# Kernel tuning notes

Hardware: AMD Instinct MI355X
Metric: run time of the kernel (lower is better)

## Reference

```python
import jax, jax.numpy as jnp
import numpy as np

N_NODES = 100000
N_EDGES = 600000
FEAT = 128
N_RELS = 8


def setup_inputs() -> dict:
    key = jax.random.key(0)
    k1, k2, k3, k4, k5, k6, k7 = jax.random.split(key, 7)
    return {
        "h": jax.random.normal(k1, (N_NODES, FEAT), dtype=jnp.float32),
        "weight": jax.random.normal(k2, (N_RELS, FEAT, FEAT), dtype=jnp.float32) * (1.0 / np.sqrt(FEAT)),
        "gate_weight": jax.random.normal(k3, (N_RELS, FEAT, 1), dtype=jnp.float32) * (1.0 / np.sqrt(FEAT)),
        "norm": jax.random.uniform(k4, (N_EDGES, 1), dtype=jnp.float32),
        "src": jax.random.randint(k5, (N_EDGES,), 0, N_NODES, dtype=jnp.int32),
        "dst": jax.random.randint(k6, (N_EDGES,), 0, N_NODES, dtype=jnp.int32),
        "rel_type": jax.random.randint(k7, (N_EDGES,), 0, N_RELS, dtype=jnp.int32),
    }


def reference(h, weight, gate_weight, norm, src, dst, rel_type):
    # Transform every node by every relation once: [N, R, F].
    # Mathematically identical to per-edge bmm h_src @ W[rel], but avoids
    # materializing an [E, F, F] gathered weight tensor.
    h_all = jnp.einsum('nd,rdf->nrf', h, weight)            # [N, R, F]
    gate_all = jnp.einsum('nd,rdo->nro', h, gate_weight)[..., 0]  # [N, R]

    msg = h_all[src, rel_type] * norm                        # [E, F]
    gate = jax.nn.sigmoid(gate_all[src, rel_type])[:, None]  # [E, 1]
    msg = msg * gate

    out = jax.ops.segment_sum(msg, dst, num_segments=h.shape[0])  # scatter-sum to dst nodes
    return jax.nn.relu(out)
```

## Files before the change

kernel.cpp:

```cpp
#include <hip/hip_runtime.h>
#include <hip/hip_bf16.h>

#define FEAT 128
#define NRELS 8
#define KTOT 1024
#define BN 32
#define SCAN2 1024

typedef __bf16 bf16_t;
typedef __bf16 bf16x2_t __attribute__((ext_vector_type(2)));
typedef __bf16 bf16x4_t __attribute__((ext_vector_type(4)));
typedef __bf16 bf16x8_t __attribute__((ext_vector_type(8)));
typedef float f32x4 __attribute__((ext_vector_type(4)));

struct __align__(8) PackedEdge { int row; float scale; };

static inline size_t align256(size_t x) { return (x + 255) & ~(size_t)255; }

__global__ void k_convert_w2(const float* __restrict__ w, bf16_t* __restrict__ wt2) {
    int i = blockIdx.x * blockDim.x + threadIdx.x;
    if (i >= NRELS * FEAT * FEAT) return;
    int r = i >> 14;
    int rem = i & 16383;
    int d = rem >> 7;
    int f = rem & 127;
    wt2[(size_t)f * KTOT + r * FEAT + d] = (bf16_t)w[i];
}

__global__ __launch_bounds__(256) void k_prep(const float* __restrict__ h,
                                              const float* __restrict__ gw,
                                              float* __restrict__ sg,
                                              bf16_t* __restrict__ hb, int ncount) {
    int wv = (int)((blockIdx.x * blockDim.x + threadIdx.x) >> 6);
    int lane = threadIdx.x & 63;
    if (wv >= ncount) return;

    float2 hv2 = *reinterpret_cast<const float2*>(h + (size_t)wv * FEAT + lane * 2);
    bf16x2_t hc;
    hc.x = (bf16_t)hv2.x;
    hc.y = (bf16_t)hv2.y;
    *reinterpret_cast<bf16x2_t*>(hb + (size_t)wv * FEAT + lane * 2) = hc;

    int r = lane >> 3;
    int g = lane & 7;
    const float4* hp = reinterpret_cast<const float4*>(h + (size_t)wv * FEAT + g * 16);
    const float4* wp = reinterpret_cast<const float4*>(gw + r * FEAT + g * 16);
    float s = 0.f;
#pragma unroll
    for (int i = 0; i < 4; ++i) {
        float4 a = hp[i];
        float4 b = wp[i];
        s += a.x * b.x + a.y * b.y + a.z * b.z + a.w * b.w;
    }
    s += __shfl_xor(s, 1, 64);
    s += __shfl_xor(s, 2, 64);
    s += __shfl_xor(s, 4, 64);
    if (g == 0) sg[(size_t)wv * NRELS + r] = 1.0f / (1.0f + __expf(-s));
}

__global__ void k_degree8(const int* __restrict__ dstv, const int* __restrict__ rel,
                          int* __restrict__ deg8, int nedges) {
    int e = blockIdx.x * blockDim.x + threadIdx.x;
    if (e >= nedges) return;
    atomicAdd(&deg8[(dstv[e] << 3) | rel[e]], 1);
}

__global__ __launch_bounds__(1024) void k_scan_block2(const int* __restrict__ in,
                                                      int* __restrict__ outv,
                                                      int* __restrict__ bsum, int n) {
    __shared__ int sm[1024];
    int t = threadIdx.x;
    int idx = blockIdx.x * SCAN2 + t;
    int v = (idx < n) ? in[idx] : 0;
    sm[t] = v;
    __syncthreads();
    for (int off = 1; off < 1024; off <<= 1) {
        int x = (t >= off) ? sm[t - off] : 0;
        __syncthreads();
        sm[t] += x;
        __syncthreads();
    }
    if (idx < n) outv[idx] = sm[t] - v;
    if (t == 1023) bsum[blockIdx.x] = sm[1023];
}

__global__ __launch_bounds__(1024) void k_scan_tops(int* __restrict__ bsum, int nb,
                                                    int* __restrict__ rowptr_end) {
    __shared__ int sm[1024];
    int t = threadIdx.x;
    if (nb <= 1024) {
        int v = (t < nb) ? bsum[t] : 0;
        sm[t] = v;
        __syncthreads();
        for (int off = 1; off < 1024; off <<= 1) {
            int x = (t >= off) ? sm[t - off] : 0;
            __syncthreads();
            sm[t] += x;
            __syncthreads();
        }
        if (t < nb) bsum[t] = sm[t] - v;
        if (t == 1023) *rowptr_end = sm[1023];
    } else if (t == 0) {
        int run = 0;
        for (int b = 0; b < nb; ++b) { int v = bsum[b]; bsum[b] = run; run += v; }
        *rowptr_end = run;
    }
}

__global__ void k_scan_add2(int* __restrict__ rowptr, const int* __restrict__ bsum,
                            int* __restrict__ wcur, int n) {
    int i = blockIdx.x * blockDim.x + threadIdx.x;
    if (i >= n) return;
    int v = rowptr[i] + bsum[i >> 10];
    rowptr[i] = v;
    wcur[i] = v;
}

__global__ void k_fill8(const int* __restrict__ src, const int* __restrict__ dstv,
                        const int* __restrict__ rel, const float* __restrict__ nrm,
                        const float* __restrict__ sg, int* __restrict__ wcur,
                        PackedEdge* __restrict__ packed, int nedges) {
    int e = blockIdx.x * blockDim.x + threadIdx.x;
    if (e >= nedges) return;
    int d = dstv[e];
    int s = src[e];
    int r = rel[e];
    int pos = atomicAdd(&wcur[(d << 3) | r], 1);
    PackedEdge p;
    p.row = (s << 3) | r;
    p.scale = nrm[e] * sg[(size_t)s * NRELS + r];
    packed[pos] = p;
}

__global__ __launch_bounds__(512, 4) void k_aggemm(const bf16_t* __restrict__ hb,
                                                   const bf16_t* __restrict__ wt2,
                                                   const PackedEdge* __restrict__ packed,
                                                   const int* __restrict__ rp8,
                                                   float* __restrict__ out, int nnodes) {
    __shared__ __align__(16) char lds_raw[BN * KTOT * sizeof(bf16_t)];
    float* cst = (float*)lds_raw;
    const int t = threadIdx.x;
    const int nb0 = blockIdx.x * BN;

    {
        f32x4 z = {0.f, 0.f, 0.f, 0.f};
#pragma unroll
        for (int i = 0; i < 8; ++i)
            reinterpret_cast<f32x4*>(lds_raw)[t + i * 512] = z;
    }
    __syncthreads();

    {
        const int g = t >> 4;
        const int il = t & 15;
        const int sw = g & 7;
        const int gnode = nb0 + g;
        int beg = 0, end = 0;
        if (gnode < nnodes) {
            beg = rp8[gnode * 8];
            end = rp8[gnode * 8 + 8];
        }

        if (beg < end) {
            float a[8];
#pragma unroll
            for (int i = 0; i < 8; ++i) a[i] = 0.f;
            int cur_r;

            auto ldrow = [&](const PackedEdge& p) {
                return *reinterpret_cast<const bf16x8_t*>(
                    hb + ((size_t)(p.row >> 3) << 7) + il * 8);
            };
            auto flush = [&](int rr) {
                bf16x8_t o;
#pragma unroll
                for (int i = 0; i < 8; ++i) o[i] = (bf16_t)a[i];
                int chunk = (rr * 16 + il) ^ sw;
                *reinterpret_cast<bf16x8_t*>(lds_raw + (size_t)g * 2048 + chunk * 16) = o;
            };
            auto consume = [&](const PackedEdge& p, const bf16x8_t& v, int idx) {
                if (idx < end) {
                    int r = p.row & 7;
                    if (r != cur_r) {
                        flush(cur_r);
#pragma unroll
                        for (int i = 0; i < 8; ++i) a[i] = 0.f;
                        cur_r = r;
                    }
                    float s = p.scale;
#pragma unroll
                    for (int i = 0; i < 8; ++i) a[i] += (float)v[i] * s;
                }
            };

            int j = beg;
            PackedEdge p0, p1, p2, p3, q0, q1, q2, q3;
            p0 = packed[j];
            p1 = (j + 1 < end) ? packed[j + 1] : p0;
            p2 = (j + 2 < end) ? packed[j + 2] : p0;
            p3 = (j + 3 < end) ? packed[j + 3] : p0;
            q0 = (j + 4 < end) ? packed[j + 4] : p0;
            q1 = (j + 5 < end) ? packed[j + 5] : p0;
            q2 = (j + 6 < end) ? packed[j + 6] : p0;
            q3 = (j + 7 < end) ? packed[j + 7] : p0;
            bf16x8_t v0 = ldrow(p0);
            bf16x8_t v1 = ldrow(p1);
            bf16x8_t v2 = ldrow(p2);
            bf16x8_t v3 = ldrow(p3);
            cur_r = p0.row & 7;

#pragma unroll 1
            for (; j < end; j += 4) {
                PackedEdge r0 = p0, r1 = p0, r2 = p0, r3 = p0;
                if (j + 8 < end)  r0 = packed[j + 8];
                if (j + 9 < end)  r1 = packed[j + 9];
                if (j + 10 < end) r2 = packed[j + 10];
                if (j + 11 < end) r3 = packed[j + 11];

                consume(p0, v0, j);
                consume(p1, v1, j + 1);
                consume(p2, v2, j + 2);
                consume(p3, v3, j + 3);

                v0 = ldrow(q0); v1 = ldrow(q1); v2 = ldrow(q2); v3 = ldrow(q3);
                p0 = q0; p1 = q1; p2 = q2; p3 = q3;
                q0 = r0; q1 = r1; q2 = r2; q3 = r3;
            }
            flush(cur_r);
        }
    }
    __syncthreads();

    const int lane = t & 63;
    const int wv = t >> 6;
    const int l15 = lane & 15;
    const int lhi = lane >> 4;
    f32x4 acc0 = {0.f, 0.f, 0.f, 0.f};
    f32x4 acc1 = {0.f, 0.f, 0.f, 0.f};
    const bf16_t* bp = wt2 + (size_t)(wv * 16 + l15) * KTOT + lhi * 8;
    const char* a0p = lds_raw + (size_t)l15 * 2048;
    const char* a1p = a0p + 16 * 2048;
    const int sw = l15 & 7;
#pragma unroll 4
    for (int ks = 0; ks < 32; ++ks) {
        int coff = ((ks * 4 + lhi) ^ sw) << 4;
        bf16x8_t av0 = *reinterpret_cast<const bf16x8_t*>(a0p + coff);
        bf16x8_t av1 = *reinterpret_cast<const bf16x8_t*>(a1p + coff);
        bf16x8_t bv = *reinterpret_cast<const bf16x8_t*>(bp + ks * 32);
        acc0 = __builtin_amdgcn_mfma_f32_16x16x32_bf16(av0, bv, acc0, 0, 0, 0);
        acc1 = __builtin_amdgcn_mfma_f32_16x16x32_bf16(av1, bv, acc1, 0, 0, 0);
    }
    __syncthreads();

    {
        int f = wv * 16 + l15;
#pragma unroll
        for (int i = 0; i < 4; ++i) {
            int n0 = lhi * 4 + i;
            cst[n0 * 132 + f] = acc0[i];
            cst[(n0 + 16) * 132 + f] = acc1[i];
        }
    }
    __syncthreads();

    {
        int node = t >> 4;
        int f0 = (t & 15) * 8;
        int gnode = nb0 + node;
        if (gnode < nnodes) {
            const float* cr = cst + node * 132 + f0;
            float4 o0, o1;
            o0.x = fmaxf(cr[0], 0.f); o0.y = fmaxf(cr[1], 0.f);
            o0.z = fmaxf(cr[2], 0.f); o0.w = fmaxf(cr[3], 0.f);
            o1.x = fmaxf(cr[4], 0.f); o1.y = fmaxf(cr[5], 0.f);
            o1.z = fmaxf(cr[6], 0.f); o1.w = fmaxf(cr[7], 0.f);
            float4* op = reinterpret_cast<float4*>(out + (size_t)gnode * FEAT + f0);
            op[0] = o0;
            op[1] = o1;
        }
    }
}

extern "C" void kernel_launch(void* const* d_in, const int* in_sizes, int n_in,
                              void* d_out, int out_size, void* d_ws, size_t ws_size,
                              hipStream_t stream) {
    const float* h = (const float*)d_in[0];
    const float* w = (const float*)d_in[1];
    const float* gw = (const float*)d_in[2];
    const float* nrm = (const float*)d_in[3];
    const int* src = (const int*)d_in[4];
    const int* dst = (const int*)d_in[5];
    const int* rel = (const int*)d_in[6];
    float* out = (float*)d_out;

    const int N = in_sizes[0] / FEAT;
    const int E = in_sizes[4];
    const int NSEG = N * NRELS;
    const int nb2 = (NSEG + SCAN2 - 1) / SCAN2;
    const int nbk = (N + BN - 1) / BN;

    char* ws = (char*)d_ws;
    const size_t wt2B = align256((size_t)FEAT * KTOT * sizeof(bf16_t));
    const size_t hbB  = align256((size_t)N * FEAT * sizeof(bf16_t));
    const size_t sgB  = align256((size_t)N * NRELS * sizeof(float));
    const size_t dgB  = align256((size_t)NSEG * sizeof(int));
    const size_t rpB  = align256((size_t)(NSEG + 1) * sizeof(int));
    const size_t bsB  = align256((size_t)nb2 * sizeof(int));

    bf16_t* wt2 = (bf16_t*)ws;
    bf16_t* hb = (bf16_t*)(ws + wt2B);
    float* sg = (float*)(ws + wt2B + hbB);
    int* deg8 = (int*)(ws + wt2B + hbB + sgB);
    int* rp8 = (int*)(ws + wt2B + hbB + sgB + dgB);
    int* bsum = (int*)(ws + wt2B + hbB + sgB + dgB + rpB);
    PackedEdge* packed = (PackedEdge*)(ws + wt2B + hbB + sgB + dgB + rpB + bsB);

    k_convert_w2<<<(NRELS * FEAT * FEAT + 255) / 256, 256, 0, stream>>>(w, wt2);
    k_prep<<<(N + 3) / 4, 256, 0, stream>>>(h, gw, sg, hb, N);

    hipMemsetAsync(deg8, 0, (size_t)NSEG * sizeof(int), stream);
    k_degree8<<<(E + 255) / 256, 256, 0, stream>>>(dst, rel, deg8, E);
    k_scan_block2<<<nb2, 1024, 0, stream>>>(deg8, rp8, bsum, NSEG);
    k_scan_tops<<<1, 1024, 0, stream>>>(bsum, nb2, rp8 + NSEG);
    k_scan_add2<<<(NSEG + 255) / 256, 256, 0, stream>>>(rp8, bsum, deg8, NSEG);
    k_fill8<<<(E + 255) / 256, 256, 0, stream>>>(src, dst, rel, nrm, sg, deg8,
                                                 packed, E);

    k_aggemm<<<nbk, 512, 0, stream>>>(hb, wt2, packed, rp8, out, N);
}
```

Before: 346.6 us.

## Bucket edges per 32-node block and sort in LDS inside aggregation kernel

Replaces the per-(node,relation) CSR build, a multi-kernel scan over 800k segments, with a coarse per-block bucket count (N/32 buckets), a single-block scan and a fill. The aggregation kernel then does a counting sort of each block's edges into (node,relation) order in shared memory. Prep, degree counting and weight conversion are merged into one launch, and the B-fragment loads in the MFMA loop are software-pipelined. This cuts launch count and global scan traffic, at the cost of extra LDS work and atomics in the main kernel. Flushes now read-modify-write bf16 in LDS across edge chunks, which can lose a little precision.

```diff
diff --git a/kernel.cpp b/kernel.cpp
--- a/kernel.cpp
+++ b/kernel.cpp
@@ -5,11 +5,10 @@
 #define NRELS 8
 #define KTOT 1024
 #define BN 32
-#define SCAN2 1024
+#define ECAP 512
 
 typedef __bf16 bf16_t;
 typedef __bf16 bf16x2_t __attribute__((ext_vector_type(2)));
-typedef __bf16 bf16x4_t __attribute__((ext_vector_type(4)));
 typedef __bf16 bf16x8_t __attribute__((ext_vector_type(8)));
 typedef float f32x4 __attribute__((ext_vector_type(4)));
 
@@ -17,79 +16,67 @@
 
 static inline size_t align256(size_t x) { return (x + 255) & ~(size_t)255; }
 
-__global__ void k_convert_w2(const float* __restrict__ w, bf16_t* __restrict__ wt2) {
-    int i = blockIdx.x * blockDim.x + threadIdx.x;
-    if (i >= NRELS * FEAT * FEAT) return;
-    int r = i >> 14;
-    int rem = i & 16383;
-    int d = rem >> 7;
-    int f = rem & 127;
-    wt2[(size_t)f * KTOT + r * FEAT + d] = (bf16_t)w[i];
-}
-
-__global__ __launch_bounds__(256) void k_prep(const float* __restrict__ h,
-                                              const float* __restrict__ gw,
-                                              float* __restrict__ sg,
-                                              bf16_t* __restrict__ hb, int ncount) {
-    int wv = (int)((blockIdx.x * blockDim.x + threadIdx.x) >> 6);
-    int lane = threadIdx.x & 63;
-    if (wv >= ncount) return;
-
-    float2 hv2 = *reinterpret_cast<const float2*>(h + (size_t)wv * FEAT + lane * 2);
-    bf16x2_t hc;
-    hc.x = (bf16_t)hv2.x;
-    hc.y = (bf16_t)hv2.y;
-    *reinterpret_cast<bf16x2_t*>(hb + (size_t)wv * FEAT + lane * 2) = hc;
-
-    int r = lane >> 3;
-    int g = lane & 7;
-    const float4* hp = reinterpret_cast<const float4*>(h + (size_t)wv * FEAT + g * 16);
-    const float4* wp = reinterpret_cast<const float4*>(gw + r * FEAT + g * 16);
-    float s = 0.f;
-#pragma unroll
-    for (int i = 0; i < 4; ++i) {
-        float4 a = hp[i];
-        float4 b = wp[i];
-        s += a.x * b.x + a.y * b.y + a.z * b.z + a.w * b.w;
-    }
-    s += __shfl_xor(s, 1, 64);
-    s += __shfl_xor(s, 2, 64);
-    s += __shfl_xor(s, 4, 64);
-    if (g == 0) sg[(size_t)wv * NRELS + r] = 1.0f / (1.0f + __expf(-s));
-}
-
-__global__ void k_degree8(const int* __restrict__ dstv, const int* __restrict__ rel,
-                          int* __restrict__ deg8, int nedges) {
-    int e = blockIdx.x * blockDim.x + threadIdx.x;
-    if (e >= nedges) return;
-    atomicAdd(&deg8[(dstv[e] << 3) | rel[e]], 1);
-}
-
-__global__ __launch_bounds__(1024) void k_scan_block2(const int* __restrict__ in,
-                                                      int* __restrict__ outv,
-                                                      int* __restrict__ bsum, int n) {
+__global__ __launch_bounds__(256) void k_phase1(const float* __restrict__ h,
+                                                const float* __restrict__ gw,
+                                                const int* __restrict__ dstv,
+                                                const float* __restrict__ w,
+                                                float* __restrict__ sg,
+                                                bf16_t* __restrict__ hb,
+                                                int* __restrict__ degb,
+                                                bf16_t* __restrict__ wt2,
+                                                int nprep, int ndeg, int N, int E) {
+    const int b = blockIdx.x;
+    const int t = threadIdx.x;
+    if (b < nprep) {
+        int wv = b * 4 + (t >> 6);
+        int lane = t & 63;
+        if (wv >= N) return;
+        float2 hv2 = *reinterpret_cast<const float2*>(h + (size_t)wv * FEAT + lane * 2);
+        bf16x2_t hc;
+        hc.x = (bf16_t)hv2.x;
+        hc.y = (bf16_t)hv2.y;
+        *reinterpret_cast<bf16x2_t*>(hb + (size_t)wv * FEAT + lane * 2) = hc;
+
+        int r = lane >> 3;
+        int g = lane & 7;
+        const float4* hp = reinterpret_cast<const float4*>(h + (size_t)wv * FEAT + g * 16);
+        const float4* wp = reinterpret_cast<const float4*>(gw + r * FEAT + g * 16);
+        float s = 0.f;
+#pragma unroll
+        for (int i = 0; i < 4; ++i) {
+            float4 a = hp[i];
+            float4 bb = wp[i];
+            s += a.x * bb.x + a.y * bb.y + a.z * bb.z + a.w * bb.w;
+        }
+        s += __shfl_xor(s, 1, 64);
+        s += __shfl_xor(s, 2, 64);
+        s += __shfl_xor(s, 4, 64);
+        if (g == 0) sg[(size_t)wv * NRELS + r] = 1.0f / (1.0f + __expf(-s));
+    } else if (b < nprep + ndeg) {
+        int e = (b - nprep) * 256 + t;
+        if (e < E) atomicAdd(&degb[dstv[e] >> 5], 1);
+    } else {
+        int i = (b - nprep - ndeg) * 256 + t;
+        if (i < NRELS * FEAT * FEAT) {
+            int r = i >> 14;
+            int rem = i & 16383;
+            int d = rem >> 7;
+            int f = rem & 127;
+            wt2[(size_t)f * KTOT + r * FEAT + d] = (bf16_t)w[i];
+        }
+    }
+}
+
+__global__ __launch_bounds__(1024) void k_scan_one(const int* __restrict__ deg,
+                                                   int* __restrict__ base,
+                                                   int* __restrict__ cur, int nb) {
     __shared__ int sm[1024];
+    __shared__ int carry;
     int t = threadIdx.x;
-    int idx = blockIdx.x * SCAN2 + t;
-    int v = (idx < n) ? in[idx] : 0;
-    sm[t] = v;
+    if (t == 0) carry = 0;
     __syncthreads();
-    for (int off = 1; off < 1024; off <<= 1) {
-        int x = (t >= off) ? sm[t - off] : 0;
-        __syncthreads();
-        sm[t] += x;
-        __syncthreads();
-    }
-    if (idx < n) outv[idx] = sm[t] - v;
-    if (t == 1023) bsum[blockIdx.x] = sm[1023];
-}
-
-__global__ __launch_bounds__(1024) void k_scan_tops(int* __restrict__ bsum, int nb,
-                                                    int* __restrict__ rowptr_end) {
-    __shared__ int sm[1024];
-    int t = threadIdx.x;
-    if (nb <= 1024) {
-        int v = (t < nb) ? bsum[t] : 0;
+    for (int s0 = 0; s0 < nb; s0 += 1024) {
+        int v = (s0 + t < nb) ? deg[s0 + t] : 0;
         sm[t] = v;
         __syncthreads();
         for (int off = 1; off < 1024; off <<= 1) {
@@ -98,36 +85,31 @@
             sm[t] += x;
             __syncthreads();
         }
-        if (t < nb) bsum[t] = sm[t] - v;
-        if (t == 1023) *rowptr_end = sm[1023];
-    } else if (t == 0) {
-        int run = 0;
-        for (int b = 0; b < nb; ++b) { int v = bsum[b]; bsum[b] = run; run += v; }
-        *rowptr_end = run;
-    }
-}
-
-__global__ void k_scan_add2(int* __restrict__ rowptr, const int* __restrict__ bsum,
-                            int* __restrict__ wcur, int n) {
-    int i = blockIdx.x * blockDim.x + threadIdx.x;
-    if (i >= n) return;
-    int v = rowptr[i] + bsum[i >> 10];
-    rowptr[i] = v;
-    wcur[i] = v;
-}
-
-__global__ void k_fill8(const int* __restrict__ src, const int* __restrict__ dstv,
+        if (s0 + t < nb) {
+            int ex = carry + sm[t] - v;
+            base[s0 + t] = ex;
+            cur[s0 + t] = ex;
+        }
+        int tot = sm[1023];
+        __syncthreads();
+        if (t == 0) carry += tot;
+        __syncthreads();
+    }
+    if (t == 0) base[nb] = carry;
+}
+
+__global__ void k_fillb(const int* __restrict__ src, const int* __restrict__ dstv,
                         const int* __restrict__ rel, const float* __restrict__ nrm,
-                        const float* __restrict__ sg, int* __restrict__ wcur,
+                        const float* __restrict__ sg, int* __restrict__ cur,
                         PackedEdge* __restrict__ packed, int nedges) {
     int e = blockIdx.x * blockDim.x + threadIdx.x;
     if (e >= nedges) return;
     int d = dstv[e];
     int s = src[e];
     int r = rel[e];
-    int pos = atomicAdd(&wcur[(d << 3) | r], 1);
+    int pos = atomicAdd(&cur[d >> 5], 1);
     PackedEdge p;
-    p.row = (s << 3) | r;
+    p.row = (s << 8) | ((d & 31) << 3) | r;
     p.scale = nrm[e] * sg[(size_t)s * NRELS + r];
     packed[pos] = p;
 }
@@ -135,121 +117,172 @@
 __global__ __launch_bounds__(512, 4) void k_aggemm(const bf16_t* __restrict__ hb,
                                                    const bf16_t* __restrict__ wt2,
                                                    const PackedEdge* __restrict__ packed,
-                                                   const int* __restrict__ rp8,
+                                                   const int* __restrict__ bbase,
                                                    float* __restrict__ out, int nnodes) {
     __shared__ __align__(16) char lds_raw[BN * KTOT * sizeof(bf16_t)];
+    __shared__ __align__(8) PackedEdge elist[ECAP];
+    __shared__ int kcnt[256];
+    __shared__ int kbase[257];
+    __shared__ int kwork[256];
     float* cst = (float*)lds_raw;
     const int t = threadIdx.x;
     const int nb0 = blockIdx.x * BN;
-
-    {
-        f32x4 z = {0.f, 0.f, 0.f, 0.f};
-#pragma unroll
-        for (int i = 0; i < 8; ++i)
-            reinterpret_cast<f32x4*>(lds_raw)[t + i * 512] = z;
-    }
-    __syncthreads();
-
-    {
-        const int g = t >> 4;
-        const int il = t & 15;
-        const int sw = g & 7;
-        const int gnode = nb0 + g;
-        int beg = 0, end = 0;
-        if (gnode < nnodes) {
-            beg = rp8[gnode * 8];
-            end = rp8[gnode * 8 + 8];
-        }
-
-        if (beg < end) {
-            float a[8];
-#pragma unroll
-            for (int i = 0; i < 8; ++i) a[i] = 0.f;
-            int cur_r;
-
-            auto ldrow = [&](const PackedEdge& p) {
-                return *reinterpret_cast<const bf16x8_t*>(
-                    hb + ((size_t)(p.row >> 3) << 7) + il * 8);
-            };
-            auto flush = [&](int rr) {
-                bf16x8_t o;
-#pragma unroll
-                for (int i = 0; i < 8; ++i) o[i] = (bf16_t)a[i];
-                int chunk = (rr * 16 + il) ^ sw;
-                *reinterpret_cast<bf16x8_t*>(lds_raw + (size_t)g * 2048 + chunk * 16) = o;
-            };
-            auto consume = [&](const PackedEdge& p, const bf16x8_t& v, int idx) {
-                if (idx < end) {
-                    int r = p.row & 7;
-                    if (r != cur_r) {
-                        flush(cur_r);
-#pragma unroll
-                        for (int i = 0; i < 8; ++i) a[i] = 0.f;
-                        cur_r = r;
-                    }
-                    float s = p.scale;
-#pragma unroll
-                    for (int i = 0; i < 8; ++i) a[i] += (float)v[i] * s;
-                }
-            };
-
-            int j = beg;
-            PackedEdge p0, p1, p2, p3, q0, q1, q2, q3;
-            p0 = packed[j];
-            p1 = (j + 1 < end) ? packed[j + 1] : p0;
-            p2 = (j + 2 < end) ? packed[j + 2] : p0;
-            p3 = (j + 3 < end) ? packed[j + 3] : p0;
-            q0 = (j + 4 < end) ? packed[j + 4] : p0;
-            q1 = (j + 5 < end) ? packed[j + 5] : p0;
-            q2 = (j + 6 < end) ? packed[j + 6] : p0;
-            q3 = (j + 7 < end) ? packed[j + 7] : p0;
-            bf16x8_t v0 = ldrow(p0);
-            bf16x8_t v1 = ldrow(p1);
-            bf16x8_t v2 = ldrow(p2);
-            bf16x8_t v3 = ldrow(p3);
-            cur_r = p0.row & 7;
-
-#pragma unroll 1
-            for (; j < end; j += 4) {
-                PackedEdge r0 = p0, r1 = p0, r2 = p0, r3 = p0;
-                if (j + 8 < end)  r0 = packed[j + 8];
-                if (j + 9 < end)  r1 = packed[j + 9];
-                if (j + 10 < end) r2 = packed[j + 10];
-                if (j + 11 < end) r3 = packed[j + 11];
-
-                consume(p0, v0, j);
-                consume(p1, v1, j + 1);
-                consume(p2, v2, j + 2);
-                consume(p3, v3, j + 3);
-
-                v0 = ldrow(q0); v1 = ldrow(q1); v2 = ldrow(q2); v3 = ldrow(q3);
-                p0 = q0; p1 = q1; p2 = q2; p3 = q3;
-                q0 = r0; q1 = r1; q2 = r2; q3 = r3;
-            }
-            flush(cur_r);
-        }
-    }
-    __syncthreads();
-
     const int lane = t & 63;
     const int wv = t >> 6;
     const int l15 = lane & 15;
     const int lhi = lane >> 4;
+
+    const bf16_t* bp = wt2 + (size_t)(wv * 16 + l15) * KTOT + lhi * 8;
+    bf16x8_t bv0 = *reinterpret_cast<const bf16x8_t*>(bp);
+    bf16x8_t bv1 = *reinterpret_cast<const bf16x8_t*>(bp + 32);
+    bf16x8_t bv2 = *reinterpret_cast<const bf16x8_t*>(bp + 64);
+    bf16x8_t bv3 = *reinterpret_cast<const bf16x8_t*>(bp + 96);
+
+    {
+        f32x4 z = {0.f, 0.f, 0.f, 0.f};
+#pragma unroll
+        for (int i = 0; i < 8; ++i)
+            reinterpret_cast<f32x4*>(lds_raw)[t + i * 512] = z;
+    }
+
+    const int ebeg = bbase[blockIdx.x];
+    const int etot = bbase[blockIdx.x + 1] - ebeg;
+
+    for (int done = 0; done < etot; done += ECAP) {
+        const int nE = min(etot - done, ECAP);
+        if (t < 256) kcnt[t] = 0;
+        __syncthreads();
+
+        PackedEdge myrec = {0, 0.f};
+        if (t < nE) {
+            myrec = packed[ebeg + done + t];
+            atomicAdd(&kcnt[myrec.row & 255], 1);
+        }
+        __syncthreads();
+
+        if (t < 64) {
+            int c0 = kcnt[t * 4], c1 = kcnt[t * 4 + 1];
+            int c2 = kcnt[t * 4 + 2], c3 = kcnt[t * 4 + 3];
+            int tot = c0 + c1 + c2 + c3;
+            int incl = tot;
+#pragma unroll
+            for (int off = 1; off < 64; off <<= 1) {
+                int y = __shfl_up(incl, off, 64);
+                if (t >= off) incl += y;
+            }
+            int excl = incl - tot;
+            kbase[t * 4] = excl;               kwork[t * 4] = excl;
+            kbase[t * 4 + 1] = excl + c0;      kwork[t * 4 + 1] = excl + c0;
+            kbase[t * 4 + 2] = excl + c0 + c1; kwork[t * 4 + 2] = excl + c0 + c1;
+            kbase[t * 4 + 3] = excl + c0 + c1 + c2;
+            kwork[t * 4 + 3] = excl + c0 + c1 + c2;
+            if (t == 63) kbase[256] = excl + tot;
+        }
+        __syncthreads();
+
+        if (t < nE) elist[atomicAdd(&kwork[myrec.row & 255], 1)] = myrec;
+        __syncthreads();
+
+        {
+            const int g = t >> 4;
+            const int il = t & 15;
+            const int sw = g & 7;
+            const int jbeg = kbase[g * 8];
+            const int jend = kbase[g * 8 + 8];
+            if (jbeg < jend) {
+                float a[8];
+#pragma unroll
+                for (int i = 0; i < 8; ++i) a[i] = 0.f;
+                int cur_r;
+
+                auto ldrec = [&](int idx) {
+                    return elist[idx < jend ? idx : jend - 1];
+                };
+                auto ldrow = [&](const PackedEdge& p) {
+                    return *reinterpret_cast<const bf16x8_t*>(
+                        hb + ((size_t)(p.row >> 8) << 7) + il * 8);
+                };
+                auto flush = [&](int rr) {
+                    int chunk = (rr * 16 + il) ^ sw;
+                    bf16_t* dp = reinterpret_cast<bf16_t*>(
+                        lds_raw + (size_t)g * 2048 + chunk * 16);
+                    bf16x8_t old = *reinterpret_cast<const bf16x8_t*>(dp);
+                    bf16x8_t o;
+#pragma unroll
+                    for (int i = 0; i < 8; ++i) o[i] = (bf16_t)((float)old[i] + a[i]);
+                    *reinterpret_cast<bf16x8_t*>(dp) = o;
+                };
+                auto consume = [&](const PackedEdge& p, const bf16x8_t& v, int idx) {
+                    if (idx < jend) {
+                        int r = p.row & 7;
+                        if (r != cur_r) {
+                            flush(cur_r);
+#pragma unroll
+                            for (int i = 0; i < 8; ++i) a[i] = 0.f;
+                            cur_r = r;
+                        }
+                        float s = p.scale;
+#pragma unroll
+                        for (int i = 0; i < 8; ++i) a[i] += (float)v[i] * s;
+                    }
+                };
+
+                PackedEdge p0 = ldrec(jbeg), p1 = ldrec(jbeg + 1);
+                PackedEdge p2 = ldrec(jbeg + 2), p3 = ldrec(jbeg + 3);
+                PackedEdge q0 = ldrec(jbeg + 4), q1 = ldrec(jbeg + 5);
+                PackedEdge q2 = ldrec(jbeg + 6), q3 = ldrec(jbeg + 7);
+                bf16x8_t v0 = ldrow(p0);
+                bf16x8_t v1 = ldrow(p1);
+                bf16x8_t v2 = ldrow(p2);
+                bf16x8_t v3 = ldrow(p3);
+                cur_r = p0.row & 7;
+
+#pragma unroll 1
+                for (int j = jbeg; j < jend; j += 4) {
+                    PackedEdge r0 = ldrec(j + 8), r1 = ldrec(j + 9);
+                    PackedEdge r2 = ldrec(j + 10), r3 = ldrec(j + 11);
+                    consume(p0, v0, j);
+                    consume(p1, v1, j + 1);
+                    consume(p2, v2, j + 2);
+                    consume(p3, v3, j + 3);
+                    v0 = ldrow(q0); v1 = ldrow(q1); v2 = ldrow(q2); v3 = ldrow(q3);
+                    p0 = q0; p1 = q1; p2 = q2; p3 = q3;
+                    q0 = r0; q1 = r1; q2 = r2; q3 = r3;
+                }
+                flush(cur_r);
+            }
+        }
+        __syncthreads();
+    }
+    __syncthreads();
+
     f32x4 acc0 = {0.f, 0.f, 0.f, 0.f};
     f32x4 acc1 = {0.f, 0.f, 0.f, 0.f};
-    const bf16_t* bp = wt2 + (size_t)(wv * 16 + l15) * KTOT + lhi * 8;
     const char* a0p = lds_raw + (size_t)l15 * 2048;
     const char* a1p = a0p + 16 * 2048;
-    const int sw = l15 & 7;
-#pragma unroll 4
-    for (int ks = 0; ks < 32; ++ks) {
-        int coff = ((ks * 4 + lhi) ^ sw) << 4;
-        bf16x8_t av0 = *reinterpret_cast<const bf16x8_t*>(a0p + coff);
-        bf16x8_t av1 = *reinterpret_cast<const bf16x8_t*>(a1p + coff);
-        bf16x8_t bv = *reinterpret_cast<const bf16x8_t*>(bp + ks * 32);
-        acc0 = __builtin_amdgcn_mfma_f32_16x16x32_bf16(av0, bv, acc0, 0, 0, 0);
-        acc1 = __builtin_amdgcn_mfma_f32_16x16x32_bf16(av1, bv, acc1, 0, 0, 0);
-    }
+    const int swb = l15 & 7;
+
+#define PB_STEP(I, BV)                                                         \
+    {                                                                          \
+        int ks = ks0 + (I);                                                    \
+        int coff = ((ks * 4 + lhi) ^ swb) << 4;                                \
+        bf16x8_t av0 = *reinterpret_cast<const bf16x8_t*>(a0p + coff);         \
+        bf16x8_t av1 = *reinterpret_cast<const bf16x8_t*>(a1p + coff);         \
+        bf16x8_t nxt = *reinterpret_cast<const bf16x8_t*>(                     \
+            bp + (((ks + 4) & 31) * 32));                                      \
+        acc0 = __builtin_amdgcn_mfma_f32_16x16x32_bf16(av0, BV, acc0, 0, 0, 0);\
+        acc1 = __builtin_amdgcn_mfma_f32_16x16x32_bf16(av1, BV, acc1, 0, 0, 0);\
+        BV = nxt;                                                              \
+    }
+
+#pragma unroll 1
+    for (int ks0 = 0; ks0 < 32; ks0 += 4) {
+        PB_STEP(0, bv0)
+        PB_STEP(1, bv1)
+        PB_STEP(2, bv2)
+        PB_STEP(3, bv3)
+    }
+#undef PB_STEP
     __syncthreads();
 
     {
@@ -295,36 +328,33 @@
 
     const int N = in_sizes[0] / FEAT;
     const int E = in_sizes[4];
-    const int NSEG = N * NRELS;
-    const int nb2 = (NSEG + SCAN2 - 1) / SCAN2;
     const int nbk = (N + BN - 1) / BN;
 
     char* ws = (char*)d_ws;
     const size_t wt2B = align256((size_t)FEAT * KTOT * sizeof(bf16_t));
     const size_t hbB  = align256((size_t)N * FEAT * sizeof(bf16_t));
     const size_t sgB  = align256((size_t)N * NRELS * sizeof(float));
-    const size_t dgB  = align256((size_t)NSEG * sizeof(int));
-    const size_t rpB  = align256((size_t)(NSEG + 1) * sizeof(int));
-    const size_t bsB  = align256((size_t)nb2 * sizeof(int));
+    const size_t dgB  = align256((size_t)nbk * sizeof(int));
+    const size_t bbB  = align256((size_t)(nbk + 1) * sizeof(int));
+    const size_t cuB  = align256((size_t)nbk * sizeof(int));
 
     bf16_t* wt2 = (bf16_t*)ws;
     bf16_t* hb = (bf16_t*)(ws + wt2B);
     float* sg = (float*)(ws + wt2B + hbB);
-    int* deg8 = (int*)(ws + wt2B + hbB + sgB);
-    int* rp8 = (int*)(ws + wt2B + hbB + sgB + dgB);
-    int* bsum = (int*)(ws + wt2B + hbB + sgB + dgB + rpB);
-    PackedEdge* packed = (PackedEdge*)(ws + wt2B + hbB + sgB + dgB + rpB + bsB);
-
-    k_convert_w2<<<(NRELS * FEAT * FEAT + 255) / 256, 256, 0, stream>>>(w, wt2);
-    k_prep<<<(N + 3) / 4, 256, 0, stream>>>(h, gw, sg, hb, N);
-
-    hipMemsetAsync(deg8, 0, (size_t)NSEG * sizeof(int), stream);
-    k_degree8<<<(E + 255) / 256, 256, 0, stream>>>(dst, rel, deg8, E);
-    k_scan_block2<<<nb2, 1024, 0, stream>>>(deg8, rp8, bsum, NSEG);
-    k_scan_tops<<<1, 1024, 0, stream>>>(bsum, nb2, rp8 + NSEG);
-    k_scan_add2<<<(NSEG + 255) / 256, 256, 0, stream>>>(rp8, bsum, deg8, NSEG);
-    k_fill8<<<(E + 255) / 256, 256, 0, stream>>>(src, dst, rel, nrm, sg, deg8,
+    int* degb = (int*)(ws + wt2B + hbB + sgB);
+    int* bbase = (int*)(ws + wt2B + hbB + sgB + dgB);
+    int* cur = (int*)(ws + wt2B + hbB + sgB + dgB + bbB);
+    PackedEdge* packed = (PackedEdge*)(ws + wt2B + hbB + sgB + dgB + bbB + cuB);
+
+    const int nprep = (N + 3) / 4;
+    const int ndeg = (E + 255) / 256;
+    const int nwcv = (NRELS * FEAT * FEAT + 255) / 256;
+
+    hipMemsetAsync(degb, 0, (size_t)nbk * sizeof(int), stream);
+    k_phase1<<<nprep + ndeg + nwcv, 256, 0, stream>>>(h, gw, dst, w, sg, hb, degb,
+                                                      wt2, nprep, ndeg, N, E);
+    k_scan_one<<<1, 1024, 0, stream>>>(degb, bbase, cur, nbk);
+    k_fillb<<<(E + 255) / 256, 256, 0, stream>>>(src, dst, rel, nrm, sg, cur,
                                                  packed, E);
-
-    k_aggemm<<<nbk, 512, 0, stream>>>(hb, wt2, packed, rp8, out, N);
-}
+    k_aggemm<<<nbk, 512, 0, stream>>>(hb, wt2, packed, bbase, out, N);
+}
```

Result: slower. 388.3 us (+12.0%).
